# Performance work log

Measured on AMD Instinct MI355X. Metric: run time of the kernel, lower is better.

## Reference

```python
import jax, jax.numpy as jnp
import numpy as np

B, T, C = 2, 2048, 1024
NH = 16
HD = C // NH

def setup_inputs() -> dict:
    key = jax.random.key(0)
    k1, k2, k3 = jax.random.split(key, 3)
    x = jax.random.normal(k1, (B, T, C), dtype=jnp.float32)
    w_attn = jax.random.normal(k2, (C, 3 * C), dtype=jnp.float32) * 0.02
    w_proj = jax.random.normal(k3, (C, C), dtype=jnp.float32) * 0.02
    return {"x": x, "w_attn": w_attn, "w_proj": w_proj}

def reference(x, w_attn, w_proj):
    b, t, c = x.shape
    qkv = x @ w_attn                                  # [B,T,3C]
    q, k, v = jnp.split(qkv, 3, axis=-1)
    # [B,NH,T,HD]
    q = q.reshape(b, t, NH, HD).transpose(0, 2, 1, 3)
    k = k.reshape(b, t, NH, HD).transpose(0, 2, 1, 3)
    v = v.reshape(b, t, NH, HD).transpose(0, 2, 1, 3)
    scale = 1.0 / np.sqrt(HD).astype(np.float32)
    att = jnp.einsum('bhqd,bhkd->bhqk', q, k) * scale  # [B,NH,T,T]
    causal = jnp.tril(jnp.ones((t, t), dtype=bool))
    att = jnp.where(causal[None, None], att, jnp.float32(-jnp.inf))
    att = jax.nn.softmax(att, axis=-1)
    y = jnp.einsum('bhqk,bhkd->bhqd', att, v)          # [B,NH,T,HD]
    y = y.transpose(0, 2, 1, 3).reshape(b, t, c)
    return y @ w_proj
```

## Files before the change

kernel.cpp:

```cpp
#include <hip/hip_runtime.h>
#include <hip/hip_bf16.h>

#define BB 2
#define TT 2048
#define CCH 1024
#define NHH 16
#define HDD 64
#define M_TOK (BB*TT)
#define N_QKV (3*CCH)

typedef __attribute__((ext_vector_type(8))) short bf16x8;
typedef __attribute__((ext_vector_type(4))) float f32x4;
typedef unsigned short u16;
typedef unsigned int u32;

__device__ __forceinline__ u16 f2bf(float f) {
    union { float f; u32 u; } v; v.f = f;
    u32 u = v.u;
    u32 r = (u + 0x7FFFu + ((u >> 16) & 1u)) >> 16;
    return (u16)r;
}

__device__ __forceinline__ u32 pk_bf16(float a, float b) {
    u32 ua = __float_as_uint(a) + 0x8000u;
    u32 ub = __float_as_uint(b) + 0x8000u;
    return __builtin_amdgcn_perm(ub, ua, 0x07060302u);
}

__device__ __forceinline__ void async_copy16(const void* g, void* l) {
    __builtin_amdgcn_global_load_lds((__attribute__((address_space(1))) void*)g,
                                     (__attribute__((address_space(3))) void*)l,
                                     16, 0, 0);
}


__global__ __launch_bounds__(256) void cast_bf16_kernel(
    const float* __restrict__ src, u16* __restrict__ dst, int n4) {
    int i = blockIdx.x * 256 + threadIdx.x;
    if (i < n4) {
        float4 f = ((const float4*)src)[i];
        ushort4 o;
        o.x = f2bf(f.x); o.y = f2bf(f.y); o.z = f2bf(f.z); o.w = f2bf(f.w);
        ((ushort4*)dst)[i] = o;
    }
}

__global__ __launch_bounds__(256) void transpose_bf16_kernel(
    const float* __restrict__ src, u16* __restrict__ dst, int R, int Cn,
    int scale_rows, float sc) {
    __shared__ float tile[32][33];
    int c0 = blockIdx.x * 32, r0 = blockIdx.y * 32;
    int tx = threadIdx.x, ty = threadIdx.y;
#pragma unroll
    for (int i = ty; i < 32; i += 8)
        tile[i][tx] = src[(size_t)(r0 + i) * Cn + c0 + tx];
    __syncthreads();
#pragma unroll
    for (int i = ty; i < 32; i += 8) {
        float v = tile[tx][i];
        if (c0 + i < scale_rows) v *= sc;
        dst[(size_t)(c0 + i) * R + r0 + tx] = f2bf(v);
    }
}


template<int SWAP, int NJ>
__device__ __forceinline__ void gemm_kloop64(
    const u16* __restrict__ A, const u16* __restrict__ Bt, int K,
    int m0, int n0, int t, u16* __restrict__ As, u16* __restrict__ Bs,
    f32x4 (&acc)[4][4])
{
    int lane = t & 63, w = t >> 6;
    int mw = (w >> 1) * 64, nw = (w & 1) * (NJ * 16);
    int mr = lane & 15, quad = lane >> 4;
    int lr = lane >> 3;
    int cswz = (lane & 7) ^ lr;

    const u16* gA[4]; u16* lA[4];
#pragma unroll
    for (int p = 0; p < 4; ++p) {
        int grp = w * 4 + p;
        gA[p] = A + (size_t)(m0 + grp * 8 + lr) * K + cswz * 8;
        lA[p] = As + ((size_t)grp * 64 + lane) * 8;
    }
    const u16* gB[4]; u16* lB[4];
#pragma unroll
    for (int p = 0; p < NJ; ++p) {
        int grp = w * NJ + p;
        gB[p] = Bt + (size_t)(n0 + grp * 8 + lr) * K + cswz * 8;
        lB[p] = Bs + ((size_t)grp * 64 + lane) * 8;
    }

    int swm = mr & 7;
    for (int k0 = 0; k0 < K; k0 += 64) {
#pragma unroll
        for (int p = 0; p < 4; ++p) async_copy16(gA[p] + k0, lA[p]);
#pragma unroll
        for (int p = 0; p < NJ; ++p) async_copy16(gB[p] + k0, lB[p]);
        __syncthreads();
#pragma unroll
        for (int kk = 0; kk < 2; ++kk) {
            bf16x8 af[4], bfr[4];
#pragma unroll
            for (int i = 0; i < 4; ++i) {
                int r = mw + i * 16 + mr;
                af[i] = *(const bf16x8*)&As[r * 64 + (((kk * 4 + quad) ^ swm) << 3)];
            }
#pragma unroll
            for (int j = 0; j < NJ; ++j) {
                int r = nw + j * 16 + mr;
                bfr[j] = *(const bf16x8*)&Bs[r * 64 + (((kk * 4 + quad) ^ swm) << 3)];
            }
#pragma unroll
            for (int i = 0; i < 4; ++i)
#pragma unroll
                for (int j = 0; j < NJ; ++j) {
                    if (SWAP)
                        acc[i][j] = __builtin_amdgcn_mfma_f32_16x16x32_bf16(bfr[j], af[i], acc[i][j], 0, 0, 0);
                    else
                        acc[i][j] = __builtin_amdgcn_mfma_f32_16x16x32_bf16(af[i], bfr[j], acc[i][j], 0, 0, 0);
                }
        }
        __syncthreads();
    }
}


__global__ __launch_bounds__(256, 3) void qkv_gemm_kernel(
    const u16* __restrict__ A, const u16* __restrict__ Bt,
    u16* __restrict__ Qo, u16* __restrict__ Ko, u16* __restrict__ Vto)
{
    __shared__ u16 As[128 * 64];
    __shared__ u16 Bs[128 * 64];
    int t = threadIdx.x;
    int m0 = blockIdx.y * 128, n0 = blockIdx.x * 128;
    int part = n0 >> 10;
    int lane = t & 63, w = t >> 6;
    int mw = (w >> 1) * 64, nw = (w & 1) * 64;
    int mr = lane & 15, quad = lane >> 4;

    f32x4 zero = {0.f, 0.f, 0.f, 0.f};
    f32x4 acc[4][4];
#pragma unroll
    for (int i = 0; i < 4; ++i)
#pragma unroll
        for (int j = 0; j < 4; ++j) acc[i][j] = zero;

    if (part < 2) {
        gemm_kloop64<1, 4>(A, Bt, CCH, m0, n0, t, As, Bs, acc);
        u16* dstp = part ? Ko : Qo;
#pragma unroll
        for (int i = 0; i < 4; ++i)
#pragma unroll
            for (int j = 0; j < 4; ++j) {
                int tok = m0 + mw + i * 16 + mr;
                int cg0 = n0 + nw + j * 16 + quad * 4;
                int cc = cg0 & 1023;
                int h = cc >> 6, d0 = cc & 63;
                int b = tok >> 11, tt = tok & 2047;
                int bh = b * NHH + h;
                uint2 o;
                o.x = pk_bf16(acc[i][j][0], acc[i][j][1]);
                o.y = pk_bf16(acc[i][j][2], acc[i][j][3]);
                *(uint2*)&dstp[((size_t)bh * TT + tt) * HDD + d0] = o;
            }
    } else {
        gemm_kloop64<0, 4>(A, Bt, CCH, m0, n0, t, As, Bs, acc);
#pragma unroll
        for (int i = 0; i < 4; ++i)
#pragma unroll
            for (int j = 0; j < 4; ++j) {
                int t0 = m0 + mw + i * 16 + quad * 4;
                int cg = n0 + nw + j * 16 + mr;
                int cc = cg & 1023;
                int h = cc >> 6, d = cc & 63;
                int b = t0 >> 11, tt0 = t0 & 2047;
                int bh = b * NHH + h;
                uint2 o;
                o.x = pk_bf16(acc[i][j][0], acc[i][j][1]);
                o.y = pk_bf16(acc[i][j][2], acc[i][j][3]);
                *(uint2*)&Vto[((size_t)bh * HDD + d) * TT + tt0] = o;
            }
    }
}


__global__ __launch_bounds__(256) void proj_gemm_kernel(
    const u16* __restrict__ A, const u16* __restrict__ Bt, float* __restrict__ Cout)
{
    __shared__ u16 As[128 * 64];
    __shared__ u16 Bs[64 * 64];
    int t = threadIdx.x;
    int m0 = blockIdx.y * 128, n0 = blockIdx.x * 64;
    int lane = t & 63, w = t >> 6;
    int mw = (w >> 1) * 64, nw = (w & 1) * 32;
    int mr = lane & 15, quad = lane >> 4;

    f32x4 zero = {0.f, 0.f, 0.f, 0.f};
    f32x4 acc[4][4];
#pragma unroll
    for (int i = 0; i < 4; ++i)
#pragma unroll
        for (int j = 0; j < 4; ++j) acc[i][j] = zero;

    gemm_kloop64<1, 2>(A, Bt, CCH, m0, n0, t, As, Bs, acc);

#pragma unroll
    for (int i = 0; i < 4; ++i)
#pragma unroll
        for (int j = 0; j < 2; ++j) {
            int tok = m0 + mw + i * 16 + mr;
            int cg0 = n0 + nw + j * 16 + quad * 4;
            float4 v;
            v.x = acc[i][j][0]; v.y = acc[i][j][1];
            v.z = acc[i][j][2]; v.w = acc[i][j][3];
            *(float4*)&Cout[(size_t)tok * CCH + cg0] = v;
        }
}


#define PSTRIDE 72

template<bool MASK>
__device__ __forceinline__ void tile_compute(
    const bf16x8 (&kf)[4][2], const bf16x8 (&vf)[4][2], u16* __restrict__ pb,
    bf16x8 qf0, bf16x8 qf1, int m, int quad, int qcol, int kv0,
    f32x4 (&o)[4], f32x4& ls)
{
    f32x4 zero = {0.f, 0.f, 0.f, 0.f};
    f32x4 st[4];
#pragma unroll
    for (int kc = 0; kc < 4; ++kc) {
        f32x4 s = __builtin_amdgcn_mfma_f32_16x16x32_bf16(kf[kc][0], qf0, zero, 0, 0, 0);
        st[kc]   = __builtin_amdgcn_mfma_f32_16x16x32_bf16(kf[kc][1], qf1, s, 0, 0, 0);
    }
#pragma unroll
    for (int kc = 0; kc < 4; ++kc) {
        float e0, e1, e2, e3;
#pragma unroll
        for (int r = 0; r < 4; ++r) {
            float v = st[kc][r];
            if (MASK && (kv0 + kc * 16 + quad * 4 + r > qcol)) v = -1e30f;
            float e = __builtin_amdgcn_exp2f(v);
            ls[r] += e;
            if (r == 0) e0 = e; else if (r == 1) e1 = e; else if (r == 2) e2 = e; else e3 = e;
        }
        uint2 pk; pk.x = pk_bf16(e0, e1); pk.y = pk_bf16(e2, e3);
        *(uint2*)&pb[m * PSTRIDE + kc * 16 + quad * 4] = pk;
    }
#pragma unroll
    for (int ks = 0; ks < 2; ++ks) {
        bf16x8 pf = *(const bf16x8*)&pb[m * PSTRIDE + ks * 32 + quad * 8];
#pragma unroll
        for (int dg = 0; dg < 4; ++dg)
            o[dg] = __builtin_amdgcn_mfma_f32_16x16x32_bf16(vf[dg][ks], pf, o[dg], 0, 0, 0);
    }
}

__global__ __launch_bounds__(256) void attn_kernel(
    const u16* __restrict__ Q, const u16* __restrict__ K,
    const u16* __restrict__ Vt, u16* __restrict__ Y)
{
    __shared__ u16 Ks[2][64 * 64];
    __shared__ u16 Vs[2][64 * 64];
    __shared__ u16 Pl[4][16 * PSTRIDE];
    int t = threadIdx.x;
    int w = t >> 6, lane = t & 63;
    int m = lane & 15, quad = lane >> 4;

    int bid = blockIdx.x;
    int head = bid & 31;
    int g = bid >> 5;
    int pr = (g < 8) ? g : 23 - g;
    int qbA = pr;
    int qbB = 31 - pr;
    int rowA = qbA * 64 + w * 16;
    int rowB = qbB * 64 + w * 16;

    const u16* qpA = Q + ((size_t)head * TT + rowA + m) * HDD + quad * 8;
    const u16* qpB = Q + ((size_t)head * TT + rowB + m) * HDD + quad * 8;
    bf16x8 qA0 = *(const bf16x8*)qpA;
    bf16x8 qA1 = *(const bf16x8*)(qpA + 32);
    bf16x8 qB0 = *(const bf16x8*)qpB;
    bf16x8 qB1 = *(const bf16x8*)(qpB + 32);

    const u16* kbase = K + (size_t)head * TT * HDD;
    const u16* vbase = Vt + (size_t)head * HDD * TT;
    u16* pb = &Pl[w][0];

    int lr = lane >> 3;
    int cg = (lane & 7) ^ lr;
    int r0 = w * 16 + lr, r1 = r0 + 8;
    int loff0 = (w * 128 + lane) * 8;
    int loff1 = (w * 128 + 64 + lane) * 8;

    f32x4 zero = {0.f, 0.f, 0.f, 0.f};
    f32x4 oA[4], oB[4], lsA = zero, lsB = zero;
#pragma unroll
    for (int dg = 0; dg < 4; ++dg) { oA[dg] = zero; oB[dg] = zero; }
    int qcolA = rowA + m, qcolB = rowB + m;
    int sw = m & 7;

    async_copy16(kbase + (size_t)r0 * 64 + cg * 8, &Ks[0][loff0]);
    async_copy16(kbase + (size_t)r1 * 64 + cg * 8, &Ks[0][loff1]);
    async_copy16(vbase + (size_t)r0 * TT + cg * 8, &Vs[0][loff0]);
    async_copy16(vbase + (size_t)r1 * TT + cg * 8, &Vs[0][loff1]);

    for (int ic = 0; ic <= qbB; ++ic) {
        int buf = ic & 1;
        int kv0 = ic << 6;
        __syncthreads();
        if (ic < qbB) {
            int nkv = kv0 + 64;
            async_copy16(kbase + (size_t)(nkv + r0) * 64 + cg * 8, &Ks[buf ^ 1][loff0]);
            async_copy16(kbase + (size_t)(nkv + r1) * 64 + cg * 8, &Ks[buf ^ 1][loff1]);
            async_copy16(vbase + (size_t)r0 * TT + nkv + cg * 8, &Vs[buf ^ 1][loff0]);
            async_copy16(vbase + (size_t)r1 * TT + nkv + cg * 8, &Vs[buf ^ 1][loff1]);
        }
        const u16* Kb = Ks[buf];
        const u16* Vb = Vs[buf];
        bf16x8 kf[4][2], vf[4][2];
#pragma unroll
        for (int kc = 0; kc < 4; ++kc) {
            int rr = kc * 16 + m;
            kf[kc][0] = *(const bf16x8*)&Kb[rr * 64 + ((quad ^ sw) << 3)];
            kf[kc][1] = *(const bf16x8*)&Kb[rr * 64 + (((quad + 4) ^ sw) << 3)];
            vf[kc][0] = *(const bf16x8*)&Vb[rr * 64 + ((quad ^ sw) << 3)];
            vf[kc][1] = *(const bf16x8*)&Vb[rr * 64 + (((quad + 4) ^ sw) << 3)];
        }
        if (ic < qbA)
            tile_compute<false>(kf, vf, pb, qA0, qA1, m, quad, qcolA, kv0, oA, lsA);
        else if (ic == qbA)
            tile_compute<true>(kf, vf, pb, qA0, qA1, m, quad, qcolA, kv0, oA, lsA);
        if (ic < qbB)
            tile_compute<false>(kf, vf, pb, qB0, qB1, m, quad, qcolB, kv0, oB, lsB);
        else
            tile_compute<true>(kf, vf, pb, qB0, qB1, m, quad, qcolB, kv0, oB, lsB);
    }

    float lA = (lsA[0] + lsA[1]) + (lsA[2] + lsA[3]);
    float lB = (lsB[0] + lsB[1]) + (lsB[2] + lsB[3]);
    lA += __shfl_xor(lA, 16, 64); lA += __shfl_xor(lA, 32, 64);
    lB += __shfl_xor(lB, 16, 64); lB += __shfl_xor(lB, 32, 64);
    float invA = 1.0f / lA, invB = 1.0f / lB;

    int b = head >> 4, h = head & 15;
    size_t roA = ((size_t)(b * TT + rowA + m)) * CCH + h * HDD;
    size_t roB = ((size_t)(b * TT + rowB + m)) * CCH + h * HDD;
#pragma unroll
    for (int dg = 0; dg < 4; ++dg) {
        uint2 ov;
        ov.x = pk_bf16(oA[dg][0] * invA, oA[dg][1] * invA);
        ov.y = pk_bf16(oA[dg][2] * invA, oA[dg][3] * invA);
        *(uint2*)&Y[roA + dg * 16 + quad * 4] = ov;
        ov.x = pk_bf16(oB[dg][0] * invB, oB[dg][1] * invB);
        ov.y = pk_bf16(oB[dg][2] * invB, oB[dg][3] * invB);
        *(uint2*)&Y[roB + dg * 16 + quad * 4] = ov;
    }
}


extern "C" void kernel_launch(void* const* d_in, const int* in_sizes, int n_in,
                              void* d_out, int out_size, void* d_ws, size_t ws_size,
                              hipStream_t stream) {
    const float* x      = (const float*)d_in[0];
    const float* w_attn = (const float*)d_in[1];
    const float* w_proj = (const float*)d_in[2];
    float* out = (float*)d_out;

    char* ws = (char*)d_ws;
    u16* x_bf   = (u16*)ws; ws += (size_t)M_TOK * CCH * 2;
    u16* wqkvT  = (u16*)ws; ws += (size_t)N_QKV * CCH * 2;
    u16* wprojT = (u16*)ws; ws += (size_t)CCH * CCH * 2;
    u16* qbuf   = (u16*)ws; ws += (size_t)BB * NHH * TT * HDD * 2;
    u16* kbuf   = (u16*)ws; ws += (size_t)BB * NHH * TT * HDD * 2;
    u16* vtb    = (u16*)ws; ws += (size_t)BB * NHH * HDD * TT * 2;
    u16* yb     = (u16*)ws; ws += (size_t)M_TOK * CCH * 2;

    const float QSC = 0.125f * 1.44269504088896f;

    cast_bf16_kernel<<<dim3(M_TOK * CCH / 4 / 256), dim3(256), 0, stream>>>(x, x_bf, M_TOK * CCH / 4);
    transpose_bf16_kernel<<<dim3(N_QKV / 32, CCH / 32), dim3(32, 8), 0, stream>>>(
        w_attn, wqkvT, CCH, N_QKV, CCH, QSC);
    transpose_bf16_kernel<<<dim3(CCH / 32, CCH / 32), dim3(32, 8), 0, stream>>>(
        w_proj, wprojT, CCH, CCH, 0, 1.0f);
    qkv_gemm_kernel<<<dim3(24, 32), dim3(256), 0, stream>>>(
        x_bf, wqkvT, qbuf, kbuf, vtb);
    attn_kernel<<<dim3(512), dim3(256), 0, stream>>>(qbuf, kbuf, vtb, yb);
    proj_gemm_kernel<<<dim3(16, 32), dim3(256), 0, stream>>>(yb, wprojT, out);
}
```

Baseline: 174.3 us.

## Split attention KV tile across wave pairs with 32-row query subtiles and LDS reduction

Each wave now handles 32 query rows (two 16-row subtiles) against one 32-key half of the KV tile, instead of 16 query rows against all 64 keys. K/V fragments in registers are halved and each is reused across two query subtiles, which cuts LDS reads per MFMA. The two key halves are combined at the end through shared memory with an extra sync. Launch bounds now ask for two blocks per CU. The exchange costs more accumulator registers, a reduction epilogue, and only half the waves doing the output stores.

```diff
diff --git a/kernel.cpp b/kernel.cpp
--- a/kernel.cpp
+++ b/kernel.cpp
@@ -219,54 +219,54 @@
 }
 
 
-#define PSTRIDE 72
+#define PST2 40
 
 template<bool MASK>
-__device__ __forceinline__ void tile_compute(
-    const bf16x8 (&kf)[4][2], const bf16x8 (&vf)[4][2], u16* __restrict__ pb,
-    bf16x8 qf0, bf16x8 qf1, int m, int quad, int qcol, int kv0,
-    f32x4 (&o)[4], f32x4& ls)
+__device__ __forceinline__ void tile2(
+    const bf16x8 (&kf)[2][2], const bf16x8 (&vf)[4], u16* __restrict__ pb,
+    const bf16x8 (&qf)[2][2], int m, int quad, int kvb, int qcol0,
+    f32x4 (&o)[2][4], f32x4 (&ls)[2])
 {
     f32x4 zero = {0.f, 0.f, 0.f, 0.f};
-    f32x4 st[4];
-#pragma unroll
-    for (int kc = 0; kc < 4; ++kc) {
-        f32x4 s = __builtin_amdgcn_mfma_f32_16x16x32_bf16(kf[kc][0], qf0, zero, 0, 0, 0);
-        st[kc]   = __builtin_amdgcn_mfma_f32_16x16x32_bf16(kf[kc][1], qf1, s, 0, 0, 0);
-    }
-#pragma unroll
-    for (int kc = 0; kc < 4; ++kc) {
-        float e0, e1, e2, e3;
-#pragma unroll
-        for (int r = 0; r < 4; ++r) {
-            float v = st[kc][r];
-            if (MASK && (kv0 + kc * 16 + quad * 4 + r > qcol)) v = -1e30f;
-            float e = __builtin_amdgcn_exp2f(v);
-            ls[r] += e;
-            if (r == 0) e0 = e; else if (r == 1) e1 = e; else if (r == 2) e2 = e; else e3 = e;
-        }
-        uint2 pk; pk.x = pk_bf16(e0, e1); pk.y = pk_bf16(e2, e3);
-        *(uint2*)&pb[m * PSTRIDE + kc * 16 + quad * 4] = pk;
-    }
-#pragma unroll
-    for (int ks = 0; ks < 2; ++ks) {
-        bf16x8 pf = *(const bf16x8*)&pb[m * PSTRIDE + ks * 32 + quad * 8];
+#pragma unroll
+    for (int ms = 0; ms < 2; ++ms) {
+#pragma unroll
+        for (int kc = 0; kc < 2; ++kc) {
+            f32x4 s  = __builtin_amdgcn_mfma_f32_16x16x32_bf16(kf[kc][0], qf[ms][0], zero, 0, 0, 0);
+            f32x4 st = __builtin_amdgcn_mfma_f32_16x16x32_bf16(kf[kc][1], qf[ms][1], s, 0, 0, 0);
+            float e0, e1, e2, e3;
+#pragma unroll
+            for (int r = 0; r < 4; ++r) {
+                float v = st[r];
+                if (MASK && (kvb + kc * 16 + quad * 4 + r > qcol0 + ms * 16)) v = -1e30f;
+                float e = __builtin_amdgcn_exp2f(v);
+                ls[ms][r] += e;
+                if (r == 0) e0 = e; else if (r == 1) e1 = e; else if (r == 2) e2 = e; else e3 = e;
+            }
+            uint2 pk; pk.x = pk_bf16(e0, e1); pk.y = pk_bf16(e2, e3);
+            *(uint2*)&pb[(ms * 16 + m) * PST2 + kc * 16 + quad * 4] = pk;
+        }
+    }
+#pragma unroll
+    for (int ms = 0; ms < 2; ++ms) {
+        bf16x8 pf = *(const bf16x8*)&pb[(ms * 16 + m) * PST2 + quad * 8];
 #pragma unroll
         for (int dg = 0; dg < 4; ++dg)
-            o[dg] = __builtin_amdgcn_mfma_f32_16x16x32_bf16(vf[dg][ks], pf, o[dg], 0, 0, 0);
-    }
-}
-
-__global__ __launch_bounds__(256) void attn_kernel(
+            o[ms][dg] = __builtin_amdgcn_mfma_f32_16x16x32_bf16(vf[dg], pf, o[ms][dg], 0, 0, 0);
+    }
+}
+
+#define SM_U16 21760
+
+__global__ __launch_bounds__(256, 2) void attn_kernel(
     const u16* __restrict__ Q, const u16* __restrict__ K,
     const u16* __restrict__ Vt, u16* __restrict__ Y)
 {
-    __shared__ u16 Ks[2][64 * 64];
-    __shared__ u16 Vs[2][64 * 64];
-    __shared__ u16 Pl[4][16 * PSTRIDE];
+    __shared__ u16 smem[SM_U16];
     int t = threadIdx.x;
     int w = t >> 6, lane = t & 63;
     int m = lane & 15, quad = lane >> 4;
+    int iq = w >> 1, kh = w & 1;
 
     int bid = blockIdx.x;
     int head = bid & 31;
@@ -274,37 +274,46 @@
     int pr = (g < 8) ? g : 23 - g;
     int qbA = pr;
     int qbB = 31 - pr;
-    int rowA = qbA * 64 + w * 16;
-    int rowB = qbB * 64 + w * 16;
-
-    const u16* qpA = Q + ((size_t)head * TT + rowA + m) * HDD + quad * 8;
-    const u16* qpB = Q + ((size_t)head * TT + rowB + m) * HDD + quad * 8;
-    bf16x8 qA0 = *(const bf16x8*)qpA;
-    bf16x8 qA1 = *(const bf16x8*)(qpA + 32);
-    bf16x8 qB0 = *(const bf16x8*)qpB;
-    bf16x8 qB1 = *(const bf16x8*)(qpB + 32);
+    int rbA = qbA * 64 + iq * 32;
+    int rbB = qbB * 64 + iq * 32;
+
+    const u16* qpA = Q + ((size_t)head * TT + rbA + m) * HDD + quad * 8;
+    const u16* qpB = Q + ((size_t)head * TT + rbB + m) * HDD + quad * 8;
+    bf16x8 qfA[2][2], qfB[2][2];
+    qfA[0][0] = *(const bf16x8*)qpA;
+    qfA[0][1] = *(const bf16x8*)(qpA + 32);
+    qfA[1][0] = *(const bf16x8*)(qpA + 16 * HDD);
+    qfA[1][1] = *(const bf16x8*)(qpA + 16 * HDD + 32);
+    qfB[0][0] = *(const bf16x8*)qpB;
+    qfB[0][1] = *(const bf16x8*)(qpB + 32);
+    qfB[1][0] = *(const bf16x8*)(qpB + 16 * HDD);
+    qfB[1][1] = *(const bf16x8*)(qpB + 16 * HDD + 32);
 
     const u16* kbase = K + (size_t)head * TT * HDD;
     const u16* vbase = Vt + (size_t)head * HDD * TT;
-    u16* pb = &Pl[w][0];
+    u16* pb = smem + 16384 + w * (32 * PST2);
 
     int lr = lane >> 3;
     int cg = (lane & 7) ^ lr;
     int r0 = w * 16 + lr, r1 = r0 + 8;
     int loff0 = (w * 128 + lane) * 8;
-    int loff1 = (w * 128 + 64 + lane) * 8;
+    int loff1 = loff0 + 512;
 
     f32x4 zero = {0.f, 0.f, 0.f, 0.f};
-    f32x4 oA[4], oB[4], lsA = zero, lsB = zero;
-#pragma unroll
-    for (int dg = 0; dg < 4; ++dg) { oA[dg] = zero; oB[dg] = zero; }
-    int qcolA = rowA + m, qcolB = rowB + m;
+    f32x4 oA[2][4], oB[2][4], lsA[2], lsB[2];
+#pragma unroll
+    for (int ms = 0; ms < 2; ++ms) {
+        lsA[ms] = zero; lsB[ms] = zero;
+#pragma unroll
+        for (int dg = 0; dg < 4; ++dg) { oA[ms][dg] = zero; oB[ms][dg] = zero; }
+    }
+    int qcA = rbA + m, qcB = rbB + m;
     int sw = m & 7;
 
-    async_copy16(kbase + (size_t)r0 * 64 + cg * 8, &Ks[0][loff0]);
-    async_copy16(kbase + (size_t)r1 * 64 + cg * 8, &Ks[0][loff1]);
-    async_copy16(vbase + (size_t)r0 * TT + cg * 8, &Vs[0][loff0]);
-    async_copy16(vbase + (size_t)r1 * TT + cg * 8, &Vs[0][loff1]);
+    async_copy16(kbase + (size_t)r0 * 64 + cg * 8, smem + loff0);
+    async_copy16(kbase + (size_t)r1 * 64 + cg * 8, smem + loff1);
+    async_copy16(vbase + (size_t)r0 * TT + cg * 8, smem + 8192 + loff0);
+    async_copy16(vbase + (size_t)r1 * TT + cg * 8, smem + 8192 + loff1);
 
     for (int ic = 0; ic <= qbB; ++ic) {
         int buf = ic & 1;
@@ -312,50 +321,101 @@
         __syncthreads();
         if (ic < qbB) {
             int nkv = kv0 + 64;
-            async_copy16(kbase + (size_t)(nkv + r0) * 64 + cg * 8, &Ks[buf ^ 1][loff0]);
-            async_copy16(kbase + (size_t)(nkv + r1) * 64 + cg * 8, &Ks[buf ^ 1][loff1]);
-            async_copy16(vbase + (size_t)r0 * TT + nkv + cg * 8, &Vs[buf ^ 1][loff0]);
-            async_copy16(vbase + (size_t)r1 * TT + nkv + cg * 8, &Vs[buf ^ 1][loff1]);
-        }
-        const u16* Kb = Ks[buf];
-        const u16* Vb = Vs[buf];
-        bf16x8 kf[4][2], vf[4][2];
-#pragma unroll
-        for (int kc = 0; kc < 4; ++kc) {
-            int rr = kc * 16 + m;
+            u16* dK = smem + (buf ^ 1) * 4096;
+            u16* dV = smem + 8192 + (buf ^ 1) * 4096;
+            async_copy16(kbase + (size_t)(nkv + r0) * 64 + cg * 8, dK + loff0);
+            async_copy16(kbase + (size_t)(nkv + r1) * 64 + cg * 8, dK + loff1);
+            async_copy16(vbase + (size_t)r0 * TT + nkv + cg * 8, dV + loff0);
+            async_copy16(vbase + (size_t)r1 * TT + nkv + cg * 8, dV + loff1);
+        }
+        const u16* Kb = smem + buf * 4096;
+        const u16* Vb = smem + 8192 + buf * 4096;
+        bf16x8 kf[2][2], vf[4];
+#pragma unroll
+        for (int kc = 0; kc < 2; ++kc) {
+            int rr = kh * 32 + kc * 16 + m;
             kf[kc][0] = *(const bf16x8*)&Kb[rr * 64 + ((quad ^ sw) << 3)];
             kf[kc][1] = *(const bf16x8*)&Kb[rr * 64 + (((quad + 4) ^ sw) << 3)];
-            vf[kc][0] = *(const bf16x8*)&Vb[rr * 64 + ((quad ^ sw) << 3)];
-            vf[kc][1] = *(const bf16x8*)&Vb[rr * 64 + (((quad + 4) ^ sw) << 3)];
-        }
+        }
+#pragma unroll
+        for (int dg = 0; dg < 4; ++dg) {
+            int rr = dg * 16 + m;
+            vf[dg] = *(const bf16x8*)&Vb[rr * 64 + (((kh * 4 + quad) ^ sw) << 3)];
+        }
+        int kvb = kv0 + kh * 32;
         if (ic < qbA)
-            tile_compute<false>(kf, vf, pb, qA0, qA1, m, quad, qcolA, kv0, oA, lsA);
+            tile2<false>(kf, vf, pb, qfA, m, quad, kvb, qcA, oA, lsA);
         else if (ic == qbA)
-            tile_compute<true>(kf, vf, pb, qA0, qA1, m, quad, qcolA, kv0, oA, lsA);
+            tile2<true >(kf, vf, pb, qfA, m, quad, kvb, qcA, oA, lsA);
         if (ic < qbB)
-            tile_compute<false>(kf, vf, pb, qB0, qB1, m, quad, qcolB, kv0, oB, lsB);
+            tile2<false>(kf, vf, pb, qfB, m, quad, kvb, qcB, oB, lsB);
         else
-            tile_compute<true>(kf, vf, pb, qB0, qB1, m, quad, qcolB, kv0, oB, lsB);
-    }
-
-    float lA = (lsA[0] + lsA[1]) + (lsA[2] + lsA[3]);
-    float lB = (lsB[0] + lsB[1]) + (lsB[2] + lsB[3]);
-    lA += __shfl_xor(lA, 16, 64); lA += __shfl_xor(lA, 32, 64);
-    lB += __shfl_xor(lB, 16, 64); lB += __shfl_xor(lB, 32, 64);
-    float invA = 1.0f / lA, invB = 1.0f / lB;
-
-    int b = head >> 4, h = head & 15;
-    size_t roA = ((size_t)(b * TT + rowA + m)) * CCH + h * HDD;
-    size_t roB = ((size_t)(b * TT + rowB + m)) * CCH + h * HDD;
-#pragma unroll
-    for (int dg = 0; dg < 4; ++dg) {
-        uint2 ov;
-        ov.x = pk_bf16(oA[dg][0] * invA, oA[dg][1] * invA);
-        ov.y = pk_bf16(oA[dg][2] * invA, oA[dg][3] * invA);
-        *(uint2*)&Y[roA + dg * 16 + quad * 4] = ov;
-        ov.x = pk_bf16(oB[dg][0] * invB, oB[dg][1] * invB);
-        ov.y = pk_bf16(oB[dg][2] * invB, oB[dg][3] * invB);
-        *(uint2*)&Y[roB + dg * 16 + quad * 4] = ov;
+            tile2<true >(kf, vf, pb, qfB, m, quad, kvb, qcB, oB, lsB);
+    }
+
+    float lv[2][2];
+#pragma unroll
+    for (int p = 0; p < 2; ++p)
+#pragma unroll
+        for (int ms = 0; ms < 2; ++ms) {
+            f32x4 L = p ? lsB[ms] : lsA[ms];
+            float l = (L[0] + L[1]) + (L[2] + L[3]);
+            l += __shfl_xor(l, 16, 64);
+            l += __shfl_xor(l, 32, 64);
+            lv[p][ms] = l;
+        }
+
+    __syncthreads();
+    f32x4* ob = (f32x4*)smem;
+    float* lb = (float*)&smem[21504];
+    if (kh) {
+        f32x4* dst = ob + (size_t)iq * 1024 + lane;
+#pragma unroll
+        for (int ms = 0; ms < 2; ++ms)
+#pragma unroll
+            for (int dg = 0; dg < 4; ++dg) {
+                dst[((0 + ms) * 4 + dg) * 64] = oA[ms][dg];
+                dst[((2 + ms) * 4 + dg) * 64] = oB[ms][dg];
+            }
+        if (quad == 0) {
+#pragma unroll
+            for (int ms = 0; ms < 2; ++ms) {
+                lb[(iq * 4 + 0 + ms) * 16 + m] = lv[0][ms];
+                lb[(iq * 4 + 2 + ms) * 16 + m] = lv[1][ms];
+            }
+        }
+    }
+    __syncthreads();
+    if (!kh) {
+        f32x4* src = ob + (size_t)iq * 1024 + lane;
+        float lA[2], lB[2];
+#pragma unroll
+        for (int ms = 0; ms < 2; ++ms) {
+#pragma unroll
+            for (int dg = 0; dg < 4; ++dg) {
+                oA[ms][dg] += src[((0 + ms) * 4 + dg) * 64];
+                oB[ms][dg] += src[((2 + ms) * 4 + dg) * 64];
+            }
+            lA[ms] = lv[0][ms] + lb[(iq * 4 + 0 + ms) * 16 + m];
+            lB[ms] = lv[1][ms] + lb[(iq * 4 + 2 + ms) * 16 + m];
+        }
+        int b = head >> 4, h = head & 15;
+#pragma unroll
+        for (int ms = 0; ms < 2; ++ms) {
+            float invA = 1.0f / lA[ms], invB = 1.0f / lB[ms];
+            size_t roA = ((size_t)(b * TT + rbA + ms * 16 + m)) * CCH + h * HDD;
+            size_t roB = ((size_t)(b * TT + rbB + ms * 16 + m)) * CCH + h * HDD;
+#pragma unroll
+            for (int dg = 0; dg < 4; ++dg) {
+                uint2 ov;
+                ov.x = pk_bf16(oA[ms][dg][0] * invA, oA[ms][dg][1] * invA);
+                ov.y = pk_bf16(oA[ms][dg][2] * invA, oA[ms][dg][3] * invA);
+                *(uint2*)&Y[roA + dg * 16 + quad * 4] = ov;
+                ov.x = pk_bf16(oB[ms][dg][0] * invB, oB[ms][dg][1] * invB);
+                ov.y = pk_bf16(oB[ms][dg][2] * invB, oB[ms][dg][3] * invB);
+                *(uint2*)&Y[roB + dg * 16 + quad * 4] = ov;
+            }
+        }
     }
 }
 
```

Measured after the change: 173.7 us. About the same (-0.4%).

## Split attention KV tile across two waves per query strip with LDS reduction

Applied to the files above, without the earlier changes.

Doubles the attention block to 512 threads, so each 16-row query strip is handled by two waves that each take half of the 64-key tile (32 keys each). Partial outputs and row sums from the second wave are combined through shared memory at the end, and K/V tile loads are now spread over eight waves. The aim is more waves in flight per CU and shorter per-wave dependency chains. In exchange it adds an extra barrier and an LDS reduction, and each wave still loads a full set of V fragments per tile.

```diff
diff --git a/kernel.cpp b/kernel.cpp
--- a/kernel.cpp
+++ b/kernel.cpp
@@ -219,54 +219,48 @@
 }
 
 
-#define PSTRIDE 72
+#define PST2 40
 
 template<bool MASK>
-__device__ __forceinline__ void tile_compute(
-    const bf16x8 (&kf)[4][2], const bf16x8 (&vf)[4][2], u16* __restrict__ pb,
-    bf16x8 qf0, bf16x8 qf1, int m, int quad, int qcol, int kv0,
+__device__ __forceinline__ void tile3(
+    const bf16x8 (&kf)[2][2], const bf16x8 (&vf)[4], u16* __restrict__ pb,
+    bf16x8 qf0, bf16x8 qf1, int m, int quad, int kvb, int qcol,
     f32x4 (&o)[4], f32x4& ls)
 {
     f32x4 zero = {0.f, 0.f, 0.f, 0.f};
-    f32x4 st[4];
-#pragma unroll
-    for (int kc = 0; kc < 4; ++kc) {
-        f32x4 s = __builtin_amdgcn_mfma_f32_16x16x32_bf16(kf[kc][0], qf0, zero, 0, 0, 0);
-        st[kc]   = __builtin_amdgcn_mfma_f32_16x16x32_bf16(kf[kc][1], qf1, s, 0, 0, 0);
-    }
-#pragma unroll
-    for (int kc = 0; kc < 4; ++kc) {
+#pragma unroll
+    for (int kc = 0; kc < 2; ++kc) {
+        f32x4 s  = __builtin_amdgcn_mfma_f32_16x16x32_bf16(kf[kc][0], qf0, zero, 0, 0, 0);
+        f32x4 st = __builtin_amdgcn_mfma_f32_16x16x32_bf16(kf[kc][1], qf1, s, 0, 0, 0);
         float e0, e1, e2, e3;
 #pragma unroll
         for (int r = 0; r < 4; ++r) {
-            float v = st[kc][r];
-            if (MASK && (kv0 + kc * 16 + quad * 4 + r > qcol)) v = -1e30f;
+            float v = st[r];
+            if (MASK && (kvb + kc * 16 + quad * 4 + r > qcol)) v = -1e30f;
             float e = __builtin_amdgcn_exp2f(v);
             ls[r] += e;
             if (r == 0) e0 = e; else if (r == 1) e1 = e; else if (r == 2) e2 = e; else e3 = e;
         }
         uint2 pk; pk.x = pk_bf16(e0, e1); pk.y = pk_bf16(e2, e3);
-        *(uint2*)&pb[m * PSTRIDE + kc * 16 + quad * 4] = pk;
-    }
-#pragma unroll
-    for (int ks = 0; ks < 2; ++ks) {
-        bf16x8 pf = *(const bf16x8*)&pb[m * PSTRIDE + ks * 32 + quad * 8];
-#pragma unroll
-        for (int dg = 0; dg < 4; ++dg)
-            o[dg] = __builtin_amdgcn_mfma_f32_16x16x32_bf16(vf[dg][ks], pf, o[dg], 0, 0, 0);
-    }
-}
-
-__global__ __launch_bounds__(256) void attn_kernel(
+        *(uint2*)&pb[m * PST2 + kc * 16 + quad * 4] = pk;
+    }
+    bf16x8 pf = *(const bf16x8*)&pb[m * PST2 + quad * 8];
+#pragma unroll
+    for (int dg = 0; dg < 4; ++dg)
+        o[dg] = __builtin_amdgcn_mfma_f32_16x16x32_bf16(vf[dg], pf, o[dg], 0, 0, 0);
+}
+
+#define SM_U16 26880
+
+__global__ __launch_bounds__(512, 4) void attn_kernel(
     const u16* __restrict__ Q, const u16* __restrict__ K,
     const u16* __restrict__ Vt, u16* __restrict__ Y)
 {
-    __shared__ u16 Ks[2][64 * 64];
-    __shared__ u16 Vs[2][64 * 64];
-    __shared__ u16 Pl[4][16 * PSTRIDE];
+    __shared__ __align__(16) u16 smem[SM_U16];
     int t = threadIdx.x;
     int w = t >> 6, lane = t & 63;
     int m = lane & 15, quad = lane >> 4;
+    int iq = w >> 1, kh = w & 1;
 
     int bid = blockIdx.x;
     int head = bid & 31;
@@ -274,11 +268,11 @@
     int pr = (g < 8) ? g : 23 - g;
     int qbA = pr;
     int qbB = 31 - pr;
-    int rowA = qbA * 64 + w * 16;
-    int rowB = qbB * 64 + w * 16;
-
-    const u16* qpA = Q + ((size_t)head * TT + rowA + m) * HDD + quad * 8;
-    const u16* qpB = Q + ((size_t)head * TT + rowB + m) * HDD + quad * 8;
+    int rbA = qbA * 64 + iq * 16;
+    int rbB = qbB * 64 + iq * 16;
+
+    const u16* qpA = Q + ((size_t)head * TT + rbA + m) * HDD + quad * 8;
+    const u16* qpB = Q + ((size_t)head * TT + rbB + m) * HDD + quad * 8;
     bf16x8 qA0 = *(const bf16x8*)qpA;
     bf16x8 qA1 = *(const bf16x8*)(qpA + 32);
     bf16x8 qB0 = *(const bf16x8*)qpB;
@@ -286,25 +280,23 @@
 
     const u16* kbase = K + (size_t)head * TT * HDD;
     const u16* vbase = Vt + (size_t)head * HDD * TT;
-    u16* pb = &Pl[w][0];
+    u16* pbA = smem + 16384 + (w * 2 + 0) * (16 * PST2);
+    u16* pbB = smem + 16384 + (w * 2 + 1) * (16 * PST2);
 
     int lr = lane >> 3;
     int cg = (lane & 7) ^ lr;
-    int r0 = w * 16 + lr, r1 = r0 + 8;
-    int loff0 = (w * 128 + lane) * 8;
-    int loff1 = (w * 128 + 64 + lane) * 8;
+    int r0 = w * 8 + lr;
+    int loff = (w * 64 + lane) * 8;
 
     f32x4 zero = {0.f, 0.f, 0.f, 0.f};
     f32x4 oA[4], oB[4], lsA = zero, lsB = zero;
 #pragma unroll
     for (int dg = 0; dg < 4; ++dg) { oA[dg] = zero; oB[dg] = zero; }
-    int qcolA = rowA + m, qcolB = rowB + m;
+    int qcA = rbA + m, qcB = rbB + m;
     int sw = m & 7;
 
-    async_copy16(kbase + (size_t)r0 * 64 + cg * 8, &Ks[0][loff0]);
-    async_copy16(kbase + (size_t)r1 * 64 + cg * 8, &Ks[0][loff1]);
-    async_copy16(vbase + (size_t)r0 * TT + cg * 8, &Vs[0][loff0]);
-    async_copy16(vbase + (size_t)r1 * TT + cg * 8, &Vs[0][loff1]);
+    async_copy16(kbase + (size_t)r0 * 64 + cg * 8, smem + loff);
+    async_copy16(vbase + (size_t)r0 * TT + cg * 8, smem + 8192 + loff);
 
     for (int ic = 0; ic <= qbB; ++ic) {
         int buf = ic & 1;
@@ -312,50 +304,81 @@
         __syncthreads();
         if (ic < qbB) {
             int nkv = kv0 + 64;
-            async_copy16(kbase + (size_t)(nkv + r0) * 64 + cg * 8, &Ks[buf ^ 1][loff0]);
-            async_copy16(kbase + (size_t)(nkv + r1) * 64 + cg * 8, &Ks[buf ^ 1][loff1]);
-            async_copy16(vbase + (size_t)r0 * TT + nkv + cg * 8, &Vs[buf ^ 1][loff0]);
-            async_copy16(vbase + (size_t)r1 * TT + nkv + cg * 8, &Vs[buf ^ 1][loff1]);
-        }
-        const u16* Kb = Ks[buf];
-        const u16* Vb = Vs[buf];
-        bf16x8 kf[4][2], vf[4][2];
-#pragma unroll
-        for (int kc = 0; kc < 4; ++kc) {
-            int rr = kc * 16 + m;
+            u16* dK = smem + (buf ^ 1) * 4096;
+            u16* dV = smem + 8192 + (buf ^ 1) * 4096;
+            async_copy16(kbase + (size_t)(nkv + r0) * 64 + cg * 8, dK + loff);
+            async_copy16(vbase + (size_t)r0 * TT + nkv + cg * 8, dV + loff);
+        }
+        const u16* Kb = smem + buf * 4096;
+        const u16* Vb = smem + 8192 + buf * 4096;
+        bf16x8 kf[2][2], vf[4];
+#pragma unroll
+        for (int kc = 0; kc < 2; ++kc) {
+            int rr = kh * 32 + kc * 16 + m;
             kf[kc][0] = *(const bf16x8*)&Kb[rr * 64 + ((quad ^ sw) << 3)];
             kf[kc][1] = *(const bf16x8*)&Kb[rr * 64 + (((quad + 4) ^ sw) << 3)];
-            vf[kc][0] = *(const bf16x8*)&Vb[rr * 64 + ((quad ^ sw) << 3)];
-            vf[kc][1] = *(const bf16x8*)&Vb[rr * 64 + (((quad + 4) ^ sw) << 3)];
-        }
+        }
+#pragma unroll
+        for (int dg = 0; dg < 4; ++dg) {
+            int rr = dg * 16 + m;
+            vf[dg] = *(const bf16x8*)&Vb[rr * 64 + (((kh * 4 + quad) ^ sw) << 3)];
+        }
+        int kvb = kv0 + kh * 32;
         if (ic < qbA)
-            tile_compute<false>(kf, vf, pb, qA0, qA1, m, quad, qcolA, kv0, oA, lsA);
+            tile3<false>(kf, vf, pbA, qA0, qA1, m, quad, kvb, qcA, oA, lsA);
         else if (ic == qbA)
-            tile_compute<true>(kf, vf, pb, qA0, qA1, m, quad, qcolA, kv0, oA, lsA);
+            tile3<true >(kf, vf, pbA, qA0, qA1, m, quad, kvb, qcA, oA, lsA);
         if (ic < qbB)
-            tile_compute<false>(kf, vf, pb, qB0, qB1, m, quad, qcolB, kv0, oB, lsB);
+            tile3<false>(kf, vf, pbB, qB0, qB1, m, quad, kvb, qcB, oB, lsB);
         else
-            tile_compute<true>(kf, vf, pb, qB0, qB1, m, quad, qcolB, kv0, oB, lsB);
+            tile3<true >(kf, vf, pbB, qB0, qB1, m, quad, kvb, qcB, oB, lsB);
     }
 
     float lA = (lsA[0] + lsA[1]) + (lsA[2] + lsA[3]);
     float lB = (lsB[0] + lsB[1]) + (lsB[2] + lsB[3]);
     lA += __shfl_xor(lA, 16, 64); lA += __shfl_xor(lA, 32, 64);
     lB += __shfl_xor(lB, 16, 64); lB += __shfl_xor(lB, 32, 64);
-    float invA = 1.0f / lA, invB = 1.0f / lB;
-
-    int b = head >> 4, h = head & 15;
-    size_t roA = ((size_t)(b * TT + rowA + m)) * CCH + h * HDD;
-    size_t roB = ((size_t)(b * TT + rowB + m)) * CCH + h * HDD;
-#pragma unroll
-    for (int dg = 0; dg < 4; ++dg) {
-        uint2 ov;
-        ov.x = pk_bf16(oA[dg][0] * invA, oA[dg][1] * invA);
-        ov.y = pk_bf16(oA[dg][2] * invA, oA[dg][3] * invA);
-        *(uint2*)&Y[roA + dg * 16 + quad * 4] = ov;
-        ov.x = pk_bf16(oB[dg][0] * invB, oB[dg][1] * invB);
-        ov.y = pk_bf16(oB[dg][2] * invB, oB[dg][3] * invB);
-        *(uint2*)&Y[roB + dg * 16 + quad * 4] = ov;
+
+    __syncthreads();
+    f32x4* ob = (f32x4*)smem;
+    float* lb = (float*)&smem[26624];
+    if (kh) {
+        f32x4* dst = ob + (size_t)iq * 512 + lane;
+#pragma unroll
+        for (int dg = 0; dg < 4; ++dg) {
+            dst[dg * 64] = oA[dg];
+            dst[(4 + dg) * 64] = oB[dg];
+        }
+        if (quad == 0) {
+            lb[(iq * 2 + 0) * 16 + m] = lA;
+            lb[(iq * 2 + 1) * 16 + m] = lB;
+        }
+    }
+    __syncthreads();
+    if (!kh) {
+        f32x4* src = ob + (size_t)iq * 512 + lane;
+#pragma unroll
+        for (int dg = 0; dg < 4; ++dg) {
+            oA[dg] += src[dg * 64];
+            oB[dg] += src[(4 + dg) * 64];
+        }
+        lA += lb[(iq * 2 + 0) * 16 + m];
+        lB += lb[(iq * 2 + 1) * 16 + m];
+        float invA = 1.0f / lA, invB = 1.0f / lB;
+
+        int b = head >> 4, h = head & 15;
+        size_t roA = ((size_t)(b * TT + rbA + m)) * CCH + h * HDD;
+        size_t roB = ((size_t)(b * TT + rbB + m)) * CCH + h * HDD;
+#pragma unroll
+        for (int dg = 0; dg < 4; ++dg) {
+            uint2 ov;
+            ov.x = pk_bf16(oA[dg][0] * invA, oA[dg][1] * invA);
+            ov.y = pk_bf16(oA[dg][2] * invA, oA[dg][3] * invA);
+            *(uint2*)&Y[roA + dg * 16 + quad * 4] = ov;
+            ov.x = pk_bf16(oB[dg][0] * invB, oB[dg][1] * invB);
+            ov.y = pk_bf16(oB[dg][2] * invB, oB[dg][3] * invB);
+            *(uint2*)&Y[roB + dg * 16 + quad * 4] = ov;
+        }
     }
 }
 
@@ -386,6 +409,6 @@
         w_proj, wprojT, CCH, CCH, 0, 1.0f);
     qkv_gemm_kernel<<<dim3(24, 32), dim3(256), 0, stream>>>(
         x_bf, wqkvT, qbuf, kbuf, vtb);
-    attn_kernel<<<dim3(512), dim3(256), 0, stream>>>(qbuf, kbuf, vtb, yb);
+    attn_kernel<<<dim3(512), dim3(512), 0, stream>>>(qbuf, kbuf, vtb, yb);
     proj_gemm_kernel<<<dim3(16, 32), dim3(256), 0, stream>>>(yb, wprojT, out);
 }
```

Measured after the change: 206.6 us. 18.5% more time.
